# Optimization experiments

Measured on AMD Instinct MI355X. Metric: run time of the kernel, lower is better.

Reference implementation:

```python
import jax, jax.numpy as jnp
import numpy as np

B, S, E, H = 2, 2048, 1024, 16
DH = E // H
SCALE = 1.0 / float(np.sqrt(E))  # note: original scales by 1/sqrt(hidden_dim), not head_dim


def _icl_mask(s):
    # triu(diagonal=0) is masked (-inf): only strictly-past positions visible,
    # except (0,0) which is explicitly unmasked so row 0 attends to itself.
    m = jnp.triu(jnp.ones((s, s), dtype=bool), k=0)
    return m.at[0, 0].set(False)


def setup_inputs() -> dict:
    key = jax.random.key(0)
    ks = jax.random.split(key, 7)
    mk = lambda k, shp: jax.random.normal(k, shp, dtype=jnp.float32)
    return {
        "q": mk(ks[0], (B, S, E)),
        "k": mk(ks[1], (B, S, E)),
        "v": mk(ks[2], (B, S, E)),
        "Wq": mk(ks[3], (E, E)) * 0.02,
        "Wk": mk(ks[4], (E, E)) * 0.02,
        "Wv": mk(ks[5], (E, E)) * 0.02,
        "Wo": mk(ks[6], (E, E)) * 0.02,
    }


def reference(q, k, v, Wq, Wk, Wv, Wo):
    b, s, e = q.shape
    h, dh = H, e // H
    # projections (nn.Linear: x @ W.T), split heads -> [b, h, s, dh]
    qh = (q @ Wq.T).reshape(b, s, h, dh).transpose(0, 2, 1, 3)
    kh = (k @ Wk.T).reshape(b, s, h, dh).transpose(0, 2, 1, 3)
    vh = (v @ Wv.T).reshape(b, s, h, dh).transpose(0, 2, 1, 3)
    scores = jnp.einsum("bhsd,bhtd->bhst", qh, kh) * SCALE  # [b,h,s,s]
    scores = jnp.where(_icl_mask(s), -jnp.inf, scores)
    probs = jax.nn.softmax(scores, axis=-1)
    out = jnp.einsum("bhst,bhtd->bhsd", probs, vh)
    out = out.transpose(0, 2, 1, 3).reshape(b, s, e)
    return out @ Wo.T
```

## Files before the change

kernel.cpp:

```cpp
#include <hip/hip_runtime.h>
#include <hip/hip_bf16.h>

typedef unsigned short u16;
typedef unsigned int u32;
typedef __bf16 bf16x8 __attribute__((ext_vector_type(8)));
typedef float float4_ __attribute__((ext_vector_type(4)));

#define B_ 2
#define S_ 2048
#define E_ 1024
#define H_ 16
#define DH_ 64
#define M_ (B_*S_)
#define E2_ (E_*E_)
#define SCALE_ 0.03125f
#define LOG2E_ 1.4426950408889634f

__device__ __forceinline__ u16 f2bf(float f) {
    unsigned int x = __float_as_uint(f);
    x += 0x7fffu + ((x >> 16) & 1u);
    return (u16)(x >> 16);
}

template <typename T> struct raw8;
template <> struct raw8<float> { float4_ lo, hi; };
template <> struct raw8<u16>   { bf16x8 v; };

__device__ __forceinline__ raw8<float> ldr8(const float* p) {
    raw8<float> r; const float4_* q = (const float4_*)p; r.lo = q[0]; r.hi = q[1]; return r;
}
__device__ __forceinline__ raw8<u16> ldr8(const u16* p) {
    raw8<u16> r; r.v = *(const bf16x8*)p; return r;
}
__device__ __forceinline__ bf16x8 cvt8(const raw8<u16>& r) { return r.v; }
__device__ __forceinline__ bf16x8 cvt8(const raw8<float>& r) {
    union { bf16x8 v; __hip_bfloat162 h[4]; } u;
    u.h[0] = __float22bfloat162_rn(float2{r.lo[0], r.lo[1]});
    u.h[1] = __float22bfloat162_rn(float2{r.lo[2], r.lo[3]});
    u.h[2] = __float22bfloat162_rn(float2{r.hi[0], r.hi[1]});
    u.h[3] = __float22bfloat162_rn(float2{r.hi[2], r.hi[3]});
    return u.v;
}
__device__ __forceinline__ bf16x8 ld8(const u16* p) { return *(const bf16x8*)p; }

__device__ __forceinline__ void async16(u16* lds, const u16* g) {
    __builtin_amdgcn_global_load_lds(
        (const __attribute__((address_space(1))) u32*)g,
        (__attribute__((address_space(3))) u32*)lds, 16, 0, 0);
}

__device__ __forceinline__ int swz32(int row, int col) {
    return row * 32 + ((((col >> 3) ^ (row & 3)) << 3) | (col & 7));
}

__global__ __launch_bounds__(256)
void convw_kernel(const float* __restrict__ Wq, const float* __restrict__ Wk,
                  const float* __restrict__ Wv, const float* __restrict__ Wo,
                  u16* __restrict__ Wqb, u16* __restrict__ Wkb,
                  u16* __restrict__ Wvb, u16* __restrict__ Wob) {
    const int which = blockIdx.y;
    const float* src = which == 0 ? Wq : which == 1 ? Wk : which == 2 ? Wv : Wo;
    u16* dst        = which == 0 ? Wqb : which == 1 ? Wkb : which == 2 ? Wvb : Wob;
    size_t off = ((size_t)blockIdx.x * 256 + threadIdx.x) * 8;
    *(bf16x8*)&dst[off] = cvt8(ldr8(&src[off]));
}

__global__ __launch_bounds__(256)
void convx_kernel(const float* __restrict__ q, const float* __restrict__ k,
                  const float* __restrict__ v,
                  u16* __restrict__ Xq, u16* __restrict__ Xk, u16* __restrict__ Xv) {
    const int which = blockIdx.y;
    const float* src = which == 0 ? q : which == 1 ? k : v;
    u16* dst        = which == 0 ? Xq : which == 1 ? Xk : Xv;
    size_t off = ((size_t)blockIdx.x * 256 + threadIdx.x) * 8;
    *(bf16x8*)&dst[off] = cvt8(ldr8(&src[off]));
}

__global__ __launch_bounds__(256)
void proj_kernel(const u16* __restrict__ Xq, const u16* __restrict__ Xk, const u16* __restrict__ Xv,
                 const u16* __restrict__ Wqb, const u16* __restrict__ Wkb, const u16* __restrict__ Wvb,
                 u16* __restrict__ Qh, u16* __restrict__ Kh, u16* __restrict__ Vt) {
    const int z = blockIdx.z;
    const u16* A   = (z == 0) ? Xq : (z == 1) ? Xk : Xv;
    const u16* Wb  = (z == 0) ? Wqb : (z == 1) ? Wkb : Wvb;
    u16* C         = (z == 0) ? Qh : (z == 1) ? Kh : Vt;
    const float cscale = (z == 0) ? SCALE_ : 1.0f;
    const int transV = (z == 2);
    const int bm = blockIdx.x * 128, bn = blockIdx.y * 128;

    __shared__ u16 As[2][128 * 32];
    __shared__ u16 Bs[2][128 * 32];

    const int tid  = threadIdx.x;
    const int lane = tid & 63;
    const int w    = tid >> 6;
    const int wr   = (w >> 1) * 64, wc = (w & 1) * 64;
    const int m16  = lane & 15, quad = lane >> 4, q4 = quad * 4;

    const int row0 = tid >> 2, ch = tid & 3, row1 = row0 + 64;
    const int csw  = ((ch ^ (row0 & 3)) * 8);
    const u16* ag0 = &A[(size_t)(bm + row0) * 1024 + csw];
    const u16* ag1 = &A[(size_t)(bm + row1) * 1024 + csw];
    const u16* wg0 = &Wb[(size_t)(bn + row0) * 1024 + csw];
    const u16* wg1 = &Wb[(size_t)(bn + row1) * 1024 + csw];

    float4_ acc[4][4];
#pragma unroll
    for (int i = 0; i < 4; i++)
#pragma unroll
        for (int j = 0; j < 4; j++) acc[i][j] = (float4_){0.f, 0.f, 0.f, 0.f};

    async16((u16*)((char*)As[0] + (size_t)tid * 16), ag0);
    async16((u16*)((char*)As[0] + (size_t)tid * 16 + 4096), ag1);
    async16((u16*)((char*)Bs[0] + (size_t)tid * 16), wg0);
    async16((u16*)((char*)Bs[0] + (size_t)tid * 16 + 4096), wg1);
    __syncthreads();

    auto step = [&](int t, const u16* Asc, const u16* Bsc, u16* Asn, u16* Bsn) {
        if (t < 31) {
            const size_t ko = (size_t)(t + 1) * 32;
            async16((u16*)((char*)Asn + (size_t)tid * 16), ag0 + ko);
            async16((u16*)((char*)Asn + (size_t)tid * 16 + 4096), ag1 + ko);
            async16((u16*)((char*)Bsn + (size_t)tid * 16), wg0 + ko);
            async16((u16*)((char*)Bsn + (size_t)tid * 16 + 4096), wg1 + ko);
        }
        __builtin_amdgcn_sched_barrier(0);
        bf16x8 af[4], bfr[4];
#pragma unroll
        for (int rt = 0; rt < 4; rt++)
            af[rt] = *(const bf16x8*)&Asc[swz32(wr + rt * 16 + m16, quad * 8)];
#pragma unroll
        for (int ct = 0; ct < 4; ct++)
            bfr[ct] = *(const bf16x8*)&Bsc[swz32(wc + ct * 16 + m16, quad * 8)];
#pragma unroll
        for (int rt = 0; rt < 4; rt++)
#pragma unroll
            for (int ct = 0; ct < 4; ct++)
                acc[rt][ct] = __builtin_amdgcn_mfma_f32_16x16x32_bf16(af[rt], bfr[ct], acc[rt][ct], 0, 0, 0);
        if (t < 31) __syncthreads();
    };

    for (int t = 0; t < 32; t += 2) {
        step(t,     As[0], Bs[0], As[1], Bs[1]);
        step(t + 1, As[1], Bs[1], As[0], Bs[0]);
    }

#pragma unroll
    for (int rt = 0; rt < 4; rt++)
#pragma unroll
        for (int ct = 0; ct < 4; ct++)
#pragma unroll
            for (int r = 0; r < 4; r++) {
                int row = bm + wr + rt * 16 + q4 + r;
                int col = bn + wc + ct * 16 + m16;
                u16 val = f2bf(acc[rt][ct][r] * cscale);
                if (!transV) {
                    C[(size_t)row * 1024 + col] = val;
                } else {
                    int bb = row >> 11, s = row & 2047;
                    C[((size_t)(bb * 1024 + col)) * 2048 + s] = val;
                }
            }
}

__global__ __launch_bounds__(256)
void out_kernel(const u16* __restrict__ AO, const u16* __restrict__ Wob, float* __restrict__ C) {
    const int bm = blockIdx.x * 128, bn = blockIdx.y * 64;

    __shared__ u16 As[2][128 * 32];
    __shared__ u16 Bs[2][64 * 32];

    const int tid  = threadIdx.x;
    const int lane = tid & 63;
    const int w    = tid >> 6;
    const int m16  = lane & 15, quad = lane >> 4, q4 = quad * 4;
    const int c1   = tid + 256;

    const int swc = (((tid & 3) ^ ((tid >> 2) & 3)) * 8);
    const u16* ag0 = &AO[(size_t)(bm + (tid >> 2)) * 1024 + swc];
    const u16* ag1 = &AO[(size_t)(bm + (c1 >> 2)) * 1024 + swc];
    const u16* bg  = &Wob[(size_t)(bn + (tid >> 2)) * 1024 + swc];

    float4_ acc[2][4];
#pragma unroll
    for (int i = 0; i < 2; i++)
#pragma unroll
        for (int j = 0; j < 4; j++) acc[i][j] = (float4_){0.f, 0.f, 0.f, 0.f};

    async16((u16*)((char*)As[0] + (size_t)tid * 16), ag0);
    async16((u16*)((char*)As[0] + (size_t)c1 * 16), ag1);
    async16((u16*)((char*)Bs[0] + (size_t)tid * 16), bg);
    __syncthreads();

    auto step = [&](int t, const u16* Asc, const u16* Bsc, u16* Asn, u16* Bsn) {
        if (t < 31) {
            async16((u16*)((char*)Asn + (size_t)tid * 16), ag0 + (t + 1) * 32);
            async16((u16*)((char*)Asn + (size_t)c1 * 16), ag1 + (t + 1) * 32);
            async16((u16*)((char*)Bsn + (size_t)tid * 16), bg + (t + 1) * 32);
        }
        __builtin_amdgcn_sched_barrier(0);
        bf16x8 af[2], bfr[4];
#pragma unroll
        for (int rt = 0; rt < 2; rt++)
            af[rt] = *(const bf16x8*)&Asc[swz32(w * 32 + rt * 16 + m16, quad * 8)];
#pragma unroll
        for (int ct = 0; ct < 4; ct++)
            bfr[ct] = *(const bf16x8*)&Bsc[swz32(ct * 16 + m16, quad * 8)];
#pragma unroll
        for (int rt = 0; rt < 2; rt++)
#pragma unroll
            for (int ct = 0; ct < 4; ct++)
                acc[rt][ct] = __builtin_amdgcn_mfma_f32_16x16x32_bf16(af[rt], bfr[ct], acc[rt][ct], 0, 0, 0);
        if (t < 31) __syncthreads();
    };

    for (int t = 0; t < 32; t += 2) {
        step(t,     As[0], Bs[0], As[1], Bs[1]);
        step(t + 1, As[1], Bs[1], As[0], Bs[0]);
    }

#pragma unroll
    for (int rt = 0; rt < 2; rt++)
#pragma unroll
        for (int ct = 0; ct < 4; ct++)
#pragma unroll
            for (int r = 0; r < 4; r++) {
                int row = bm + w * 32 + rt * 16 + q4 + r;
                int col = bn + ct * 16 + m16;
                C[(size_t)row * 1024 + col] = acc[rt][ct][r];
            }
}

__device__ __forceinline__ int sw64(int row, int col) {
    return row * 64 + ((((col >> 3) ^ (row & 7)) << 3) | (col & 7));
}

__global__ __launch_bounds__(256, 2)
void attn_kernel(const u16* __restrict__ Qh, const u16* __restrict__ Kh,
                 const u16* __restrict__ Vt, u16* __restrict__ O) {
    const int h    = blockIdx.x;
    const int tq   = 31 - blockIdx.y;
    const int b    = blockIdx.z;
    const int tid  = threadIdx.x;
    const int lane = tid & 63;
    const int w    = tid >> 6;
    const int m16  = lane & 15;
    const int quad = lane >> 4;
    const int q4   = quad * 4;

    __shared__ u16 Ks[3][64 * 64];
    __shared__ u16 Vs[3][64 * 64];
    __shared__ u16 Ps[64 * 64];

    const int srow0 = tid >> 3;
    const int ssw   = (((tid & 7) ^ (srow0 & 7)) * 8);

    const size_t kbase = ((size_t)(b * S_)) * E_ + h * DH_;
    const size_t vbase = ((size_t)(b * 1024 + h * DH_)) * 2048;
    const u16* kg0 = &Kh[kbase + (size_t)srow0 * E_ + ssw];
    const u16* kg1 = kg0 + (size_t)32 * E_;
    const u16* vg0 = &Vt[vbase + (size_t)srow0 * 2048 + ssw];
    const u16* vg1 = vg0 + (size_t)32 * 2048;

    bf16x8 qf[2];
    {
        const u16* qa = Qh + ((size_t)(b * S_ + tq * 64 + w * 16 + m16)) * E_ + h * DH_;
        qf[0] = ld8(qa + quad * 8);
        qf[1] = ld8(qa + 32 + quad * 8);
    }

    float l_part[4] = {0.f, 0.f, 0.f, 0.f};
    float4_ o_acc[4];
#pragma unroll
    for (int dt = 0; dt < 4; dt++) o_acc[dt] = (float4_){0.f, 0.f, 0.f, 0.f};

    u16* k0 = &Ks[0][0]; u16* k1 = &Ks[1][0]; u16* k2 = &Ks[2][0];
    u16* v0 = &Vs[0][0]; u16* v1 = &Vs[1][0]; u16* v2 = &Vs[2][0];

    auto stage_to = [&](u16* kb, u16* vb, int tile) {
        const size_t ko = (size_t)tile * 64 * E_;
        const int    vo = tile * 64;
        async16(kb + tid * 8, kg0 + ko);
        async16(kb + (tid + 256) * 8, kg1 + ko);
        async16(vb + tid * 8, vg0 + vo);
        async16(vb + (tid + 256) * 8, vg1 + vo);
    };

    stage_to(k0, v0, 0);
    stage_to(k1, v1, tq > 0 ? 1 : 0);
    asm volatile("s_waitcnt vmcnt(4)" ::: "memory");
    __builtin_amdgcn_s_barrier();
    __builtin_amdgcn_sched_barrier(0);

    for (int t = 0; t <= tq; t++) {
        stage_to(k2, v2, (t + 2 <= tq) ? (t + 2) : tq);
        __builtin_amdgcn_sched_barrier(0);

        float4_ sc[4];
#pragma unroll
        for (int ct = 0; ct < 4; ct++) sc[ct] = (float4_){0.f, 0.f, 0.f, 0.f};
#pragma unroll
        for (int ks = 0; ks < 2; ks++)
#pragma unroll
            for (int ct = 0; ct < 4; ct++) {
                bf16x8 kf = *(const bf16x8*)&k0[sw64(ct * 16 + m16, ks * 32 + quad * 8)];
                sc[ct] = __builtin_amdgcn_mfma_f32_16x16x32_bf16(qf[ks], kf, sc[ct], 0, 0, 0);
            }

#pragma unroll
        for (int ct = 0; ct < 4; ct++) {
            float pp[4];
            if (t != tq) {
#pragma unroll
                for (int r = 0; r < 4; r++) {
                    pp[r] = exp2f(sc[ct][r] * LOG2E_);
                    l_part[r] += pp[r];
                }
            } else {
#pragma unroll
                for (int r = 0; r < 4; r++) {
                    int i_loc = w * 16 + q4 + r;
                    int j_loc = ct * 16 + m16;
                    bool allow = (j_loc < i_loc) || (tq == 0 && i_loc == 0 && j_loc == 0);
                    pp[r] = allow ? exp2f(sc[ct][r] * LOG2E_) : 0.f;
                    l_part[r] += pp[r];
                }
            }
            union { __hip_bfloat162 h; u16 s[2]; } u01, u23;
            u01.h = __float22bfloat162_rn(float2{pp[0], pp[1]});
            u23.h = __float22bfloat162_rn(float2{pp[2], pp[3]});
            Ps[sw64(w * 16 + q4 + 0, ct * 16 + m16)] = u01.s[0];
            Ps[sw64(w * 16 + q4 + 1, ct * 16 + m16)] = u01.s[1];
            Ps[sw64(w * 16 + q4 + 2, ct * 16 + m16)] = u23.s[0];
            Ps[sw64(w * 16 + q4 + 3, ct * 16 + m16)] = u23.s[1];
        }

#pragma unroll
        for (int ks = 0; ks < 2; ks++) {
            bf16x8 pf = *(const bf16x8*)&Ps[sw64(w * 16 + m16, ks * 32 + quad * 8)];
#pragma unroll
            for (int dt = 0; dt < 4; dt++) {
                bf16x8 vf = *(const bf16x8*)&v0[sw64(dt * 16 + m16, ks * 32 + quad * 8)];
                o_acc[dt] = __builtin_amdgcn_mfma_f32_16x16x32_bf16(pf, vf, o_acc[dt], 0, 0, 0);
            }
        }

        asm volatile("s_waitcnt vmcnt(4)" ::: "memory");
        __builtin_amdgcn_s_barrier();
        __builtin_amdgcn_sched_barrier(0);

        u16* tk = k0; k0 = k1; k1 = k2; k2 = tk;
        u16* tv = v0; v0 = v1; v1 = v2; v2 = tv;
    }
    asm volatile("s_waitcnt vmcnt(0)" ::: "memory");

    const size_t obase = ((size_t)(b * S_ + tq * 64)) * E_ + h * DH_;
#pragma unroll
    for (int r = 0; r < 4; r++) {
        float l = l_part[r];
#pragma unroll
        for (int msk = 1; msk <= 8; msk <<= 1) l += __shfl_xor(l, msk);
        float inv_l = 1.0f / l;
        int row = w * 16 + q4 + r;
#pragma unroll
        for (int dt = 0; dt < 4; dt++) {
            int col = dt * 16 + m16;
            O[obase + (size_t)row * E_ + col] = f2bf(o_acc[dt][r] * inv_l);
        }
    }
}

extern "C" void kernel_launch(void* const* d_in, const int* in_sizes, int n_in,
                              void* d_out, int out_size, void* d_ws, size_t ws_size,
                              hipStream_t stream) {
    const float* q  = (const float*)d_in[0];
    const float* k  = (const float*)d_in[1];
    const float* v  = (const float*)d_in[2];
    const float* Wq = (const float*)d_in[3];
    const float* Wk = (const float*)d_in[4];
    const float* Wv = (const float*)d_in[5];
    const float* Wo = (const float*)d_in[6];

    const size_t ME = (size_t)M_ * E_;
    u16* ws  = (u16*)d_ws;
    u16* Qh  = ws;
    u16* Kh  = ws + ME;
    u16* Vt  = ws + 2 * ME;
    u16* AO  = ws + 3 * ME;
    u16* Wqb = AO;
    u16* Wkb = AO + E2_;
    u16* Wvb = AO + 2 * (size_t)E2_;
    u16* Wob = ws + 4 * ME;
    u16* Xv  = ws + 4 * ME + E2_;
    u16* Xq  = (u16*)d_out;
    u16* Xk  = Xq + ME;

    dim3 blk(256);
    convw_kernel<<<dim3(512, 4), blk, 0, stream>>>(Wq, Wk, Wv, Wo, Wqb, Wkb, Wvb, Wob);
    convx_kernel<<<dim3(2048, 3), blk, 0, stream>>>(q, k, v, Xq, Xk, Xv);
    proj_kernel<<<dim3(32, 8, 3), blk, 0, stream>>>(Xq, Xk, Xv, Wqb, Wkb, Wvb, Qh, Kh, Vt);
    attn_kernel<<<dim3(16, 32, 2), blk, 0, stream>>>(Qh, Kh, Vt, AO);
    out_kernel<<<dim3(32, 16), blk, 0, stream>>>(AO, Wob, (float*)d_out);
}
```

Before: 215.8 us.

## Load K/V fragments directly from global memory instead of LDS triple buffering

Removes the shared-memory triple-buffered async staging of K and V tiles and the per-iteration barriers. Each wave now loads its MFMA K and V fragments straight from global memory into registers, so all four waves of a block read the same tile redundantly and rely on cache reuse. The launch-bounds occupancy hint is also dropped. This cuts LDS traffic and block-wide synchronisation, but it increases global and cache traffic, adds register pressure, and loses the prefetch overlap.

Result: slower. 291.2 us (+34.9%).

```diff
diff --git a/kernel.cpp b/kernel.cpp
--- a/kernel.cpp
+++ b/kernel.cpp
@@ -235,7 +235,7 @@
     return row * 64 + ((((col >> 3) ^ (row & 7)) << 3) | (col & 7));
 }
 
-__global__ __launch_bounds__(256, 2)
+__global__ __launch_bounds__(256)
 void attn_kernel(const u16* __restrict__ Qh, const u16* __restrict__ Kh,
                  const u16* __restrict__ Vt, u16* __restrict__ O) {
     const int h    = blockIdx.x;
@@ -248,19 +248,12 @@
     const int quad = lane >> 4;
     const int q4   = quad * 4;
 
-    __shared__ u16 Ks[3][64 * 64];
-    __shared__ u16 Vs[3][64 * 64];
     __shared__ u16 Ps[64 * 64];
-
-    const int srow0 = tid >> 3;
-    const int ssw   = (((tid & 7) ^ (srow0 & 7)) * 8);
 
     const size_t kbase = ((size_t)(b * S_)) * E_ + h * DH_;
     const size_t vbase = ((size_t)(b * 1024 + h * DH_)) * 2048;
-    const u16* kg0 = &Kh[kbase + (size_t)srow0 * E_ + ssw];
-    const u16* kg1 = kg0 + (size_t)32 * E_;
-    const u16* vg0 = &Vt[vbase + (size_t)srow0 * 2048 + ssw];
-    const u16* vg1 = vg0 + (size_t)32 * 2048;
+    const u16* kl = Kh + kbase + (size_t)m16 * E_ + quad * 8;
+    const u16* vl = Vt + vbase + (size_t)m16 * 2048 + quad * 8;
 
     bf16x8 qf[2];
     {
@@ -274,27 +267,21 @@
 #pragma unroll
     for (int dt = 0; dt < 4; dt++) o_acc[dt] = (float4_){0.f, 0.f, 0.f, 0.f};
 
-    u16* k0 = &Ks[0][0]; u16* k1 = &Ks[1][0]; u16* k2 = &Ks[2][0];
-    u16* v0 = &Vs[0][0]; u16* v1 = &Vs[1][0]; u16* v2 = &Vs[2][0];
-
-    auto stage_to = [&](u16* kb, u16* vb, int tile) {
-        const size_t ko = (size_t)tile * 64 * E_;
-        const int    vo = tile * 64;
-        async16(kb + tid * 8, kg0 + ko);
-        async16(kb + (tid + 256) * 8, kg1 + ko);
-        async16(vb + tid * 8, vg0 + vo);
-        async16(vb + (tid + 256) * 8, vg1 + vo);
-    };
-
-    stage_to(k0, v0, 0);
-    stage_to(k1, v1, tq > 0 ? 1 : 0);
-    asm volatile("s_waitcnt vmcnt(4)" ::: "memory");
-    __builtin_amdgcn_s_barrier();
-    __builtin_amdgcn_sched_barrier(0);
-
     for (int t = 0; t <= tq; t++) {
-        stage_to(k2, v2, (t + 2 <= tq) ? (t + 2) : tq);
-        __builtin_amdgcn_sched_barrier(0);
+        const u16* kt_base = kl + (size_t)t * 64 * E_;
+        const u16* vt_base = vl + t * 64;
+
+        bf16x8 kf[4][2], vf[4][2];
+#pragma unroll
+        for (int ct = 0; ct < 4; ct++)
+#pragma unroll
+            for (int ks = 0; ks < 2; ks++)
+                kf[ct][ks] = ld8(kt_base + (size_t)(ct * 16) * E_ + ks * 32);
+#pragma unroll
+        for (int dt = 0; dt < 4; dt++)
+#pragma unroll
+            for (int ks = 0; ks < 2; ks++)
+                vf[dt][ks] = ld8(vt_base + (size_t)(dt * 16) * 2048 + ks * 32);
 
         float4_ sc[4];
 #pragma unroll
@@ -302,10 +289,8 @@
 #pragma unroll
         for (int ks = 0; ks < 2; ks++)
 #pragma unroll
-            for (int ct = 0; ct < 4; ct++) {
-                bf16x8 kf = *(const bf16x8*)&k0[sw64(ct * 16 + m16, ks * 32 + quad * 8)];
-                sc[ct] = __builtin_amdgcn_mfma_f32_16x16x32_bf16(qf[ks], kf, sc[ct], 0, 0, 0);
-            }
+            for (int ct = 0; ct < 4; ct++)
+                sc[ct] = __builtin_amdgcn_mfma_f32_16x16x32_bf16(qf[ks], kf[ct][ks], sc[ct], 0, 0, 0);
 
 #pragma unroll
         for (int ct = 0; ct < 4; ct++) {
@@ -326,9 +311,9 @@
                     l_part[r] += pp[r];
                 }
             }
-            union { __hip_bfloat162 h; u16 s[2]; } u01, u23;
-            u01.h = __float22bfloat162_rn(float2{pp[0], pp[1]});
-            u23.h = __float22bfloat162_rn(float2{pp[2], pp[3]});
+            union { __hip_bfloat162 h2; u16 s[2]; } u01, u23;
+            u01.h2 = __float22bfloat162_rn(float2{pp[0], pp[1]});
+            u23.h2 = __float22bfloat162_rn(float2{pp[2], pp[3]});
             Ps[sw64(w * 16 + q4 + 0, ct * 16 + m16)] = u01.s[0];
             Ps[sw64(w * 16 + q4 + 1, ct * 16 + m16)] = u01.s[1];
             Ps[sw64(w * 16 + q4 + 2, ct * 16 + m16)] = u23.s[0];
@@ -339,20 +324,10 @@
         for (int ks = 0; ks < 2; ks++) {
             bf16x8 pf = *(const bf16x8*)&Ps[sw64(w * 16 + m16, ks * 32 + quad * 8)];
 #pragma unroll
-            for (int dt = 0; dt < 4; dt++) {
-                bf16x8 vf = *(const bf16x8*)&v0[sw64(dt * 16 + m16, ks * 32 + quad * 8)];
-                o_acc[dt] = __builtin_amdgcn_mfma_f32_16x16x32_bf16(pf, vf, o_acc[dt], 0, 0, 0);
-            }
-        }
-
-        asm volatile("s_waitcnt vmcnt(4)" ::: "memory");
-        __builtin_amdgcn_s_barrier();
-        __builtin_amdgcn_sched_barrier(0);
-
-        u16* tk = k0; k0 = k1; k1 = k2; k2 = tk;
-        u16* tv = v0; v0 = v1; v1 = v2; v2 = tv;
-    }
-    asm volatile("s_waitcnt vmcnt(0)" ::: "memory");
+            for (int dt = 0; dt < 4; dt++)
+                o_acc[dt] = __builtin_amdgcn_mfma_f32_16x16x32_bf16(pf, vf[dt][ks], o_acc[dt], 0, 0, 0);
+        }
+    }
 
     const size_t obase = ((size_t)(b * S_ + tq * 64)) * E_ + h * DH_;
 #pragma unroll
```
